# Optimization experiments

Hardware: AMD Instinct MI355X
Metric: run time of the kernel (lower is better)

## Reference

```python
import jax, jax.numpy as jnp
import numpy as np

EPS = 1e-8  # matches init eps


def setup_inputs() -> dict:
    key = jax.random.key(0)
    ks = jax.random.split(key, 6)
    B, LA, LB, Dh, P = 2, 512, 512, 1024, 64
    return {
        "h_a": jax.random.normal(ks[0], (B, LA, Dh), dtype=jnp.float32),
        "h_b": jax.random.normal(ks[1], (B, LB, Dh), dtype=jnp.float32),
        "Wa": jax.random.normal(ks[2], (Dh, P), dtype=jnp.float32) * 0.02,
        "ba": jax.random.normal(ks[3], (P,), dtype=jnp.float32) * 0.02,
        "Wb": jax.random.normal(ks[4], (Dh, P), dtype=jnp.float32) * 0.02,
        "bb": jax.random.normal(ks[5], (P,), dtype=jnp.float32) * 0.02,
    }


def reference(h_a, h_b, Wa, ba, Wb, bb):
    # Project + exact GELU (torch default)
    z_a = jax.nn.gelu(h_a @ Wa + ba, approximate=False)  # [B,LA,P]
    z_b = jax.nn.gelu(h_b @ Wb + bb, approximate=False)  # [B,LB,P]
    B, LA, P = z_a.shape
    LB = z_b.shape[1]
    # Channel-first broadcasts: [B,P,LA,LB]
    za = jnp.transpose(z_a, (0, 2, 1))[:, :, :, None]  # [B,P,LA,1]
    zb = jnp.transpose(z_b, (0, 2, 1))[:, :, None, :]  # [B,P,1,LB]
    za_e = jnp.broadcast_to(za, (B, P, LA, LB))
    zb_e = jnp.broadcast_to(zb, (B, P, LA, LB))
    diff = jnp.abs(za_e - zb_e)
    prod = za_e * zb_e
    # cosine similarity channel, computed from per-residue stats (no D-expanded tensor)
    dot = jnp.einsum("bip,bjp->bij", z_a, z_b)[:, None]  # [B,1,LA,LB]
    na = jnp.sqrt(jnp.sum(z_a * z_a, axis=-1) + EPS)  # [B,LA]
    nb = jnp.sqrt(jnp.sum(z_b * z_b, axis=-1) + EPS)  # [B,LB]
    sim = dot / (na[:, None, :, None] * nb[:, None, None, :])
    # channel order matches torch cat([z_a, z_b, diff, prod, sim], -1).permute(0,3,1,2)
    return jnp.concatenate([za_e, zb_e, diff, prod, sim], axis=1)  # [B,4P+1,LA,LB]
```

## Files before the change

kernel.cpp:

```cpp
#include <hip/hip_runtime.h>
#include <math.h>

#define B_   2
#define LA_  512
#define LB_  512
#define DH_  1024
#define P_   64
#define NCH_ 257
#define EPS_ 1e-8f

typedef float v4f __attribute__((ext_vector_type(4)));

template <bool TRANS>
__global__ __launch_bounds__(256) void proj_gelu_kernel(
    const float* __restrict__ h,
    const float* __restrict__ W,
    const float* __restrict__ bias,
    float* __restrict__ z,
    float* __restrict__ rn,
    int L)
{
    __shared__ float hs[DH_];
    __shared__ float partial[256];

    const int row = blockIdx.x;
    const int b   = row >> 9;
    const int i   = row & (L - 1);
    const int tid = threadIdx.x;

    const float4* hrow4 = (const float4*)(h + (size_t)row * DH_);
    ((float4*)hs)[tid] = hrow4[tid];
    __syncthreads();

    const int p = tid & 63;
    const int q = tid >> 6;
    const float* Wp = W + p;
    float acc = 0.f;
    const int k0 = q * 256;
    #pragma unroll 8
    for (int k = k0; k < k0 + 256; ++k)
        acc = fmaf(hs[k], Wp[k * P_], acc);
    partial[tid] = acc;
    __syncthreads();

    if (tid < 64) {
        float v = partial[tid] + partial[tid + 64] + partial[tid + 128] +
                  partial[tid + 192] + bias[tid];
        float g = 0.5f * v * (1.f + erff(v * 0.70710678118654752f));

        if (TRANS) z[((size_t)(b * P_ + tid)) * L + i] = g;
        else       z[(size_t)row * P_ + tid] = g;

        float s = g * g;
        #pragma unroll
        for (int off = 32; off > 0; off >>= 1)
            s += __shfl_down(s, off, 64);
        if (tid == 0)
            rn[row] = 1.f / sqrtf(s + EPS_);
    }
}

__device__ __forceinline__ void nt_store4(float* p, float x, float y,
                                          float z, float w) {
    v4f v = {x, y, z, w};
    __builtin_nontemporal_store(v, (v4f*)p);
}

__global__ __launch_bounds__(128) void build_map_kernel(
    const float* __restrict__ za,
    const float* __restrict__ zbt,
    const float* __restrict__ rna,
    const float* __restrict__ rnb,
    float* __restrict__ out)
{
    __shared__ float zas[P_];

    const int idx = blockIdx.x;
    const int b   = idx >> 9;
    const int i   = idx & (LA_ - 1);
    const int tid = threadIdx.x;
    const int j0  = tid * 4;

    if (tid < P_) zas[tid] = za[(size_t)idx * P_ + tid];
    __syncthreads();

    const size_t CH = (size_t)LA_ * LB_;
    float* ob = out + (size_t)b * NCH_ * CH + (size_t)i * LB_ + j0;
    const float* zbb = zbt + (size_t)b * P_ * LB_ + j0;

    float accx = 0.f, accy = 0.f, accz = 0.f, accw = 0.f;

    #pragma unroll 4
    for (int p = 0; p < P_; ++p) {
        const float a = zas[p];
        const v4f zb = *(const v4f*)(zbb + (size_t)p * LB_);

        const float prx = a * zb.x, pry = a * zb.y,
                    prz = a * zb.z, prw = a * zb.w;
        accx += prx; accy += pry; accz += prz; accw += prw;

        nt_store4(ob + (size_t)p * CH,         a, a, a, a);
        nt_store4(ob + (size_t)(64 + p) * CH,  zb.x, zb.y, zb.z, zb.w);
        nt_store4(ob + (size_t)(128 + p) * CH, fabsf(a - zb.x), fabsf(a - zb.y),
                                               fabsf(a - zb.z), fabsf(a - zb.w));
        nt_store4(ob + (size_t)(192 + p) * CH, prx, pry, prz, prw);
    }

    const float ra = rna[idx];
    const v4f rb = *(const v4f*)(rnb + b * LB_ + j0);
    nt_store4(ob + (size_t)256 * CH,
              accx * ra * rb.x, accy * ra * rb.y,
              accz * ra * rb.z, accw * ra * rb.w);
}

extern "C" void kernel_launch(void* const* d_in, const int* in_sizes, int n_in,
                              void* d_out, int out_size, void* d_ws, size_t ws_size,
                              hipStream_t stream)
{
    const float* h_a = (const float*)d_in[0];
    const float* h_b = (const float*)d_in[1];
    const float* Wa  = (const float*)d_in[2];
    const float* ba  = (const float*)d_in[3];
    const float* Wb  = (const float*)d_in[4];
    const float* bb  = (const float*)d_in[5];
    float* out = (float*)d_out;

    float* ws  = (float*)d_ws;
    float* za  = ws;
    float* zbt = ws + (size_t)B_ * LA_ * P_;
    float* rna = zbt + (size_t)B_ * P_ * LB_;
    float* rnb = rna + (size_t)B_ * LA_;

    proj_gelu_kernel<false><<<B_ * LA_, 256, 0, stream>>>(h_a, Wa, ba, za, rna, LA_);
    proj_gelu_kernel<true ><<<B_ * LB_, 256, 0, stream>>>(h_b, Wb, bb, zbt, rnb, LB_);
    build_map_kernel<<<B_ * LA_, 128, 0, stream>>>(za, zbt, rna, rnb, out);
}
```

Measured before the change: 582.7 us.

## Split map build into per-channel writer and tiled cosine-similarity kernels

Replaces the per-row build kernel, which scattered stores across 257 channel planes, with a writer kernel that gives each block one channel plane tile and writes contiguous rows. The similarity channel moves into its own register-tiled dot-product kernel. Both projections are merged into a single launch that stores transposed z, cutting one launch. The new writer uses plain stores instead of nontemporal ones and re-reads z data per channel, so cache behaviour on the write-bound output may change.

```diff
diff --git a/kernel.cpp b/kernel.cpp
--- a/kernel.cpp
+++ b/kernel.cpp
@@ -1,35 +1,43 @@
 #include <hip/hip_runtime.h>
 #include <math.h>
 
-#define B_   2
-#define LA_  512
-#define LB_  512
-#define DH_  1024
-#define P_   64
-#define NCH_ 257
-#define EPS_ 1e-8f
+#define B_    2
+#define LA_   512
+#define LB_   512
+#define DH_   1024
+#define P_    64
+#define NCH_  257
+#define EPS_  1e-8f
+#define CH_   ((size_t)LA_ * LB_)
+#define TILES_ 4
+#define TROWS_ (LA_ / TILES_)
 
-typedef float v4f __attribute__((ext_vector_type(4)));
-
-template <bool TRANS>
 __global__ __launch_bounds__(256) void proj_gelu_kernel(
-    const float* __restrict__ h,
-    const float* __restrict__ W,
-    const float* __restrict__ bias,
-    float* __restrict__ z,
-    float* __restrict__ rn,
-    int L)
+    const float* __restrict__ h_a, const float* __restrict__ Wa,
+    const float* __restrict__ ba,
+    const float* __restrict__ h_b, const float* __restrict__ Wb,
+    const float* __restrict__ bb,
+    float* __restrict__ zat,
+    float* __restrict__ zbt,
+    float* __restrict__ rna,
+    float* __restrict__ rnb)
 {
-    __shared__ float hs[DH_];
+    __shared__ __align__(16) float hs[DH_];
     __shared__ float partial[256];
 
-    const int row = blockIdx.x;
-    const int b   = row >> 9;
-    const int i   = row & (L - 1);
-    const int tid = threadIdx.x;
+    const int side = blockIdx.x >> 10;
+    const int row  = blockIdx.x & 1023;
+    const int b    = row >> 9;
+    const int i    = row & 511;
+    const int tid  = threadIdx.x;
 
-    const float4* hrow4 = (const float4*)(h + (size_t)row * DH_);
-    ((float4*)hs)[tid] = hrow4[tid];
+    const float* h    = side ? h_b : h_a;
+    const float* W    = side ? Wb  : Wa;
+    const float* bias = side ? bb  : ba;
+    float* z  = side ? zbt : zat;
+    float* rn = side ? rnb : rna;
+
+    ((float4*)hs)[tid] = ((const float4*)(h + (size_t)row * DH_))[tid];
     __syncthreads();
 
     const int p = tid & 63;
@@ -48,8 +56,7 @@
                   partial[tid + 192] + bias[tid];
         float g = 0.5f * v * (1.f + erff(v * 0.70710678118654752f));
 
-        if (TRANS) z[((size_t)(b * P_ + tid)) * L + i] = g;
-        else       z[(size_t)row * P_ + tid] = g;
+        z[((size_t)(b * P_ + tid)) * 512 + i] = g;
 
         float s = g * g;
         #pragma unroll
@@ -60,57 +67,110 @@
     }
 }
 
-__device__ __forceinline__ void nt_store4(float* p, float x, float y,
-                                          float z, float w) {
-    v4f v = {x, y, z, w};
-    __builtin_nontemporal_store(v, (v4f*)p);
+__global__ __launch_bounds__(256) void writer_kernel(
+    const float* __restrict__ zat,
+    const float* __restrict__ zbt,
+    float* __restrict__ out)
+{
+    __shared__ __align__(16) float zbrow[LB_];
+    __shared__ __align__(16) float zacol[TROWS_];
+
+    const int ch  = blockIdx.x;
+    const int t   = ch >> 6;
+    const int p   = ch & 63;
+    const int i0  = blockIdx.y * TROWS_;
+    const int b   = blockIdx.z;
+    const int tid = threadIdx.x;
+
+    if (tid < 128)
+        ((float4*)zbrow)[tid] = ((const float4*)(zbt + (size_t)(b * P_ + p) * 512))[tid];
+    else if (tid < 160)
+        ((float4*)zacol)[tid - 128] =
+            ((const float4*)(zat + (size_t)(b * P_ + p) * 512 + i0))[tid - 128];
+    __syncthreads();
+
+    const int half = tid >> 7;
+    const int jj   = (tid & 127) * 4;
+    const float4 zbv = *(const float4*)(zbrow + jj);
+
+    float* op = out + (size_t)(b * NCH_ + ch) * CH_ + (size_t)(i0 + half) * LB_ + jj;
+
+    if (t == 0) {
+        #pragma unroll 4
+        for (int it = 0; it < TROWS_ / 2; ++it) {
+            const float a = zacol[2 * it + half];
+            *(float4*)op = make_float4(a, a, a, a);
+            op += 2 * LB_;
+        }
+    } else if (t == 1) {
+        #pragma unroll 4
+        for (int it = 0; it < TROWS_ / 2; ++it) {
+            *(float4*)op = make_float4(zbv.x, zbv.y, zbv.z, zbv.w);
+            op += 2 * LB_;
+        }
+    } else if (t == 2) {
+        #pragma unroll 4
+        for (int it = 0; it < TROWS_ / 2; ++it) {
+            const float a = zacol[2 * it + half];
+            *(float4*)op = make_float4(fabsf(a - zbv.x), fabsf(a - zbv.y),
+                                       fabsf(a - zbv.z), fabsf(a - zbv.w));
+            op += 2 * LB_;
+        }
+    } else {
+        #pragma unroll 4
+        for (int it = 0; it < TROWS_ / 2; ++it) {
+            const float a = zacol[2 * it + half];
+            *(float4*)op = make_float4(a * zbv.x, a * zbv.y, a * zbv.z, a * zbv.w);
+            op += 2 * LB_;
+        }
+    }
 }
 
-__global__ __launch_bounds__(128) void build_map_kernel(
-    const float* __restrict__ za,
+__global__ __launch_bounds__(256) void sim_kernel(
+    const float* __restrict__ zat,
     const float* __restrict__ zbt,
     const float* __restrict__ rna,
     const float* __restrict__ rnb,
     float* __restrict__ out)
 {
-    __shared__ float zas[P_];
+    __shared__ float zas[P_ * 16];
 
-    const int idx = blockIdx.x;
-    const int b   = idx >> 9;
-    const int i   = idx & (LA_ - 1);
+    const int i0  = blockIdx.x * 16;
+    const int b   = blockIdx.y;
     const int tid = threadIdx.x;
-    const int j0  = tid * 4;
 
-    if (tid < P_) zas[tid] = za[(size_t)idx * P_ + tid];
+    {
+        const int p  = tid >> 2;
+        const int ii = (tid & 3) * 4;
+        *(float4*)(zas + p * 16 + ii) =
+            *(const float4*)(zat + (size_t)(b * P_ + p) * 512 + i0 + ii);
+    }
     __syncthreads();
 
-    const size_t CH = (size_t)LA_ * LB_;
-    float* ob = out + (size_t)b * NCH_ * CH + (size_t)i * LB_ + j0;
-    const float* zbb = zbt + (size_t)b * P_ * LB_ + j0;
+    float acc0[16], acc1[16];
+    #pragma unroll
+    for (int ii = 0; ii < 16; ++ii) { acc0[ii] = 0.f; acc1[ii] = 0.f; }
 
-    float accx = 0.f, accy = 0.f, accz = 0.f, accw = 0.f;
-
-    #pragma unroll 4
     for (int p = 0; p < P_; ++p) {
-        const float a = zas[p];
-        const v4f zb = *(const v4f*)(zbb + (size_t)p * LB_);
-
-        const float prx = a * zb.x, pry = a * zb.y,
-                    prz = a * zb.z, prw = a * zb.w;
-        accx += prx; accy += pry; accz += prz; accw += prw;
-
-        nt_store4(ob + (size_t)p * CH,         a, a, a, a);
-        nt_store4(ob + (size_t)(64 + p) * CH,  zb.x, zb.y, zb.z, zb.w);
-        nt_store4(ob + (size_t)(128 + p) * CH, fabsf(a - zb.x), fabsf(a - zb.y),
-                                               fabsf(a - zb.z), fabsf(a - zb.w));
-        nt_store4(ob + (size_t)(192 + p) * CH, prx, pry, prz, prw);
+        const float zb0 = zbt[(size_t)(b * P_ + p) * 512 + tid];
+        const float zb1 = zbt[(size_t)(b * P_ + p) * 512 + tid + 256];
+        #pragma unroll
+        for (int ii = 0; ii < 16; ++ii) {
+            const float a = zas[p * 16 + ii];
+            acc0[ii] = fmaf(a, zb0, acc0[ii]);
+            acc1[ii] = fmaf(a, zb1, acc1[ii]);
+        }
     }
 
-    const float ra = rna[idx];
-    const v4f rb = *(const v4f*)(rnb + b * LB_ + j0);
-    nt_store4(ob + (size_t)256 * CH,
-              accx * ra * rb.x, accy * ra * rb.y,
-              accz * ra * rb.z, accw * ra * rb.w);
+    const float rb0 = rnb[b * 512 + tid];
+    const float rb1 = rnb[b * 512 + tid + 256];
+    float* plane = out + (size_t)(b * NCH_ + 256) * CH_;
+    #pragma unroll
+    for (int ii = 0; ii < 16; ++ii) {
+        const float ra = rna[b * 512 + i0 + ii];
+        plane[(size_t)(i0 + ii) * LB_ + tid]       = acc0[ii] * ra * rb0;
+        plane[(size_t)(i0 + ii) * LB_ + tid + 256] = acc1[ii] * ra * rb1;
+    }
 }
 
 extern "C" void kernel_launch(void* const* d_in, const int* in_sizes, int n_in,
@@ -126,12 +186,13 @@
     float* out = (float*)d_out;
 
     float* ws  = (float*)d_ws;
-    float* za  = ws;
-    float* zbt = ws + (size_t)B_ * LA_ * P_;
+    float* zat = ws;
+    float* zbt = zat + (size_t)B_ * P_ * LA_;
     float* rna = zbt + (size_t)B_ * P_ * LB_;
     float* rnb = rna + (size_t)B_ * LA_;
 
-    proj_gelu_kernel<false><<<B_ * LA_, 256, 0, stream>>>(h_a, Wa, ba, za, rna, LA_);
-    proj_gelu_kernel<true ><<<B_ * LB_, 256, 0, stream>>>(h_b, Wb, bb, zbt, rnb, LB_);
-    build_map_kernel<<<B_ * LA_, 128, 0, stream>>>(za, zbt, rna, rnb, out);
+    proj_gelu_kernel<<<2 * B_ * LA_, 256, 0, stream>>>(
+        h_a, Wa, ba, h_b, Wb, bb, zat, zbt, rna, rnb);
+    writer_kernel<<<dim3(256, TILES_, B_), 256, 0, stream>>>(zat, zbt, out);
+    sim_kernel<<<dim3(LA_ / 16, B_), 256, 0, stream>>>(zat, zbt, rna, rnb, out);
 }
```

Result: faster. 570.4 us (-2.1%).
